# Kernel tuning notes

Hardware: AMD Instinct MI355X
Metric: run time of the kernel (lower is better)

## Reference

```python
import jax, jax.numpy as jnp
import numpy as np
from jax import lax

Q = 3          # Self-ONN polynomial order
EPS = 1e-5     # InstanceNorm1d eps


def setup_inputs() -> dict:
    key = jax.random.key(0)
    k1, k2, k3 = jax.random.split(key, 3)
    B, Cin, L = 16, 128, 8192
    Cout, K = 128, 3
    x = jax.random.normal(k1, (B, Cin, L), dtype=jnp.float32)
    # Conv1d weight over power-expanded channels: [Cout, Cin*Q, K]
    W = jax.random.normal(k2, (Cout, Cin * Q, K), dtype=jnp.float32) * 0.05
    b = jax.random.normal(k3, (Cout,), dtype=jnp.float32) * 0.05
    return {"x": x, "W": W, "b": b}


def reference(x, W, b):
    x = jnp.repeat(x, 2, axis=-1)
    # Self-ONN power expansion: concat x^1..x^Q along channel dim -> (B, C*Q, 2L)
    powers = jnp.concatenate([x ** (i + 1) for i in range(Q)], axis=1)
    # Conv1d, stride 1, padding 1 (same length)
    out = lax.conv_general_dilated(
        powers, W,
        window_strides=(1,),
        padding=[(1, 1)],
        dimension_numbers=("NCH", "OIH", "NCH"),
    ) + b[None, :, None]
    # InstanceNorm1d (affine=False): normalize over length per (batch, channel)
    mean = jnp.mean(out, axis=-1, keepdims=True)
    var = jnp.var(out, axis=-1, keepdims=True)
    out = (out - mean) * lax.rsqrt(var + EPS)
    # Tanh activation (self.relu is nn.Tanh()); dropout=False -> no-op
    return jnp.tanh(out)
```

## Files before the change

### kernel.cpp

```cpp
#include <hip/hip_runtime.h>
#include <hip/hip_fp16.h>
#include <math.h>

#define BATCH 16
#define CIN   128
#define LIN   8192
#define COUT  128
#define LOUT  16384
#define KEXP  768
#define NT    128
#define NTILES (LIN/NT)
#define PCOLS 130
#define PCPAD 136
#define PSZ   (PCOLS*PCPAD)

typedef _Float16 f16x8 __attribute__((ext_vector_type(8)));
typedef float    f32x4 __attribute__((ext_vector_type(4)));

__global__ void prep_weights(const float* __restrict__ W,
                             _Float16* __restrict__ WE,
                             _Float16* __restrict__ WO) {
  int idx = blockIdx.x * 256 + threadIdx.x;
  int co = idx / KEXP;
  int k  = idx % KEXP;
  int sh = (k >= 384) ? 1 : 0;
  int cq = k - 384 * sh;
  const float* w = W + ((size_t)co * 384 + cq) * 3;
  float we, wo;
  if (sh == 0) { we = w[0];        wo = w[0] + w[1]; }
  else         { we = w[1] + w[2]; wo = w[2];        }
  int q  = cq >> 7;
  int c  = cq & 127;
  int ks = q * 8 + sh * 4 + (c >> 5);
  int kk = c & 31, quad = kk >> 3, j = kk & 7;
  int mtile = co >> 4, l15 = co & 15;
  size_t off = ((size_t)((mtile * 24 + ks) * 64) + quad * 16 + l15) * 8 + j;
  WE[off] = (_Float16)we;
  WO[off] = (_Float16)wo;
}

__launch_bounds__(512, 4)
__global__ void conv_gemm(const float* __restrict__ x,
                          const _Float16* __restrict__ WE,
                          const _Float16* __restrict__ WO,
                          float* __restrict__ out,
                          float* __restrict__ stats) {
  extern __shared__ char smem[];
  float*    sstats = (float*)smem;
  _Float16* plane  = (_Float16*)(smem + 1024);

  const int tile = blockIdx.x;
  const int b    = blockIdx.y;
  const int i0   = tile * NT;
  const int t    = threadIdx.x;
  const int lane = t & 63;
  const int wave = t >> 6;
  const int p    = wave >> 1;
  const int isO  = wave & 1;
  const int wm   = p >> 1, wn = p & 1;
  const int l15  = lane & 15, quad = lane >> 4;
  const int kl   = quad * 8;

  if (t < 128) { sstats[2 * t] = 0.f; sstats[2 * t + 1] = 0.f; }

  const float* xb = x + (size_t)b * CIN * LIN;
  const _Float16* Wsel = isO ? WO : WE;

  f32x4 acc[4][4];
  const f32x4 zero = {0.f, 0.f, 0.f, 0.f};
#pragma unroll
  for (int fm = 0; fm < 4; ++fm)
#pragma unroll
    for (int fn = 0; fn < 4; ++fn) acc[fm][fn] = zero;

#pragma unroll
  for (int q = 0; q < 3; ++q) {
    for (int task = t; task < PCOLS * 16; task += 512) {
      int g   = task / PCOLS;
      int col = task - g * PCOLS;
      int c8  = g * 8;
      int gi  = i0 - 1 + col;
      bool ok = (gi >= 0 && gi < LIN);
      f16x8 w;
#pragma unroll
      for (int j = 0; j < 8; ++j) {
        float v = ok ? xb[(size_t)(c8 + j) * LIN + gi] : 0.f;
        float pv = (q == 0) ? v : ((q == 1) ? v * v : v * v * v);
        w[j] = (_Float16)pv;
      }
      *(f16x8*)(plane + col * PCPAD + c8) = w;
    }
    __syncthreads();

#pragma unroll
    for (int s = 0; s < 8; ++s) {
      const int cb   = (s & 3) * 32;
      const int shft = (s >> 2) + isO;
      const _Float16* pb = plane + cb + kl;
      f16x8 bf[4], af[4];
#pragma unroll
      for (int fn = 0; fn < 4; ++fn) {
        int colB = wn * 64 + fn * 16 + l15 + shft;
        bf[fn] = *(const f16x8*)(pb + colB * PCPAD);
      }
#pragma unroll
      for (int fm = 0; fm < 4; ++fm) {
        int mt = wm * 4 + fm;
        af[fm] = *(const f16x8*)(Wsel + ((size_t)((mt * 24 + q * 8 + s) * 64) + lane) * 8);
      }
#pragma unroll
      for (int fm = 0; fm < 4; ++fm)
#pragma unroll
        for (int fn = 0; fn < 4; ++fn)
          acc[fm][fn] = __builtin_amdgcn_mfma_f32_16x16x32_f16(af[fm], bf[fn], acc[fm][fn], 0, 0, 0);
    }
    __syncthreads();
  }

  float* orow_base = out + (size_t)b * COUT * LOUT + isO;
#pragma unroll
  for (int fm = 0; fm < 4; ++fm) {
#pragma unroll
    for (int r = 0; r < 4; ++r) {
      float s1 = 0.f, s2 = 0.f;
#pragma unroll
      for (int fn = 0; fn < 4; ++fn) {
        float v = acc[fm][fn][r];
        s1 += v;
        s2 += v * v;
      }
#pragma unroll
      for (int off = 8; off >= 1; off >>= 1) {
        s1 += __shfl_xor(s1, off, 64);
        s2 += __shfl_xor(s2, off, 64);
      }
      int co = wm * 64 + fm * 16 + quad * 4 + r;
      if (l15 == 0) {
        atomicAdd(&sstats[2 * co], s1);
        atomicAdd(&sstats[2 * co + 1], s2);
      }
      float* orow = orow_base + (size_t)co * LOUT;
#pragma unroll
      for (int fn = 0; fn < 4; ++fn) {
        int n = i0 + wn * 64 + fn * 16 + l15;
        orow[2 * n] = acc[fm][fn][r];
      }
    }
  }
  __syncthreads();
  if (t < 128) {
    atomicAdd(&stats[((size_t)b * COUT + t) * 2],     sstats[2 * t]);
    atomicAdd(&stats[((size_t)b * COUT + t) * 2 + 1], sstats[2 * t + 1]);
  }
}

__device__ inline float tanh_fast(float z) {
  float e = __expf(2.f * z);
  return 1.f - 2.f * __builtin_amdgcn_rcpf(e + 1.f);
}

__global__ void norm_tanh(float* __restrict__ out, const float* __restrict__ stats) {
  int row = blockIdx.x;
  float s1 = stats[2 * row], s2 = stats[2 * row + 1];
  const float invN = 1.f / (float)LOUT;
  float mean = s1 * invN;
  float var  = fmaxf(s2 * invN - mean * mean, 0.f);
  float inv  = rsqrtf(var + 1e-5f);
  float c0   = -mean * inv;
  float4* p = (float4*)(out + (size_t)row * LOUT);
  for (int i = threadIdx.x; i < LOUT / 4; i += 256) {
    float4 v = p[i];
    v.x = tanh_fast(fmaf(v.x, inv, c0));
    v.y = tanh_fast(fmaf(v.y, inv, c0));
    v.z = tanh_fast(fmaf(v.z, inv, c0));
    v.w = tanh_fast(fmaf(v.w, inv, c0));
    p[i] = v;
  }
}

extern "C" void kernel_launch(void* const* d_in, const int* in_sizes, int n_in,
                              void* d_out, int out_size, void* d_ws, size_t ws_size,
                              hipStream_t stream) {
  const float* x = (const float*)d_in[0];
  const float* W = (const float*)d_in[1];
  float* out = (float*)d_out;

  float*    stats = (float*)d_ws;
  _Float16* WE    = (_Float16*)((char*)d_ws + 16384);
  _Float16* WO    = WE + (size_t)COUT * KEXP;

  hipMemsetAsync(d_ws, 0, 16384, stream);
  prep_weights<<<dim3((COUT * KEXP) / 256), dim3(256), 0, stream>>>(W, WE, WO);

  size_t shmem = 1024 + (size_t)PSZ * 2;
  hipFuncSetAttribute(reinterpret_cast<const void*>(conv_gemm),
                      hipFuncAttributeMaxDynamicSharedMemorySize, (int)shmem);
  conv_gemm<<<dim3(NTILES, BATCH), dim3(512), shmem, stream>>>(x, WE, WO, out, stats);

  norm_tanh<<<dim3(BATCH * COUT), dim3(256), 0, stream>>>(out, stats);
}
```

Baseline: 311.7 us.

## Load x once into registers and double-buffer power planes with prefetched fragments

The x tile is now read from global memory once into registers, and all three power planes are built from those registers instead of re-reading x for each power. Two LDS planes alternate, so the next power plane is written while MFMAs run on the current one. Weight and B fragments are software-prefetched (triple and double buffered), and MFMA issue priority is raised with s_setprio. This removes repeated global loads and some barriers, but raises register use (launch bounds drop to 2 blocks per CU) and doubles LDS use, which can lower occupancy.

```diff
diff --git a/kernel.cpp b/kernel.cpp
--- a/kernel.cpp
+++ b/kernel.cpp
@@ -39,7 +39,40 @@
   WO[off] = (_Float16)wo;
 }
 
-__launch_bounds__(512, 4)
+
+#define BUILD_PLANE(POW, P) do {                                           \
+  _Pragma("unroll")                                                        \
+  for (int slot = 0; slot < 5; ++slot) {                                   \
+    if (slot < 4 || tail) {                                                \
+      f16x8 w;                                                             \
+      _Pragma("unroll")                                                    \
+      for (int j = 0; j < 8; ++j) {                                        \
+        float v = xv[slot][j];                                             \
+        float pv = ((POW) == 1) ? v : (((POW) == 2) ? v * v : v * (v * v));\
+        w[j] = (_Float16)pv;                                               \
+      }                                                                    \
+      *(f16x8*)((P) + woff[slot]) = w;                                     \
+    }                                                                      \
+  }                                                                        \
+} while (0)
+
+#define AFLOAD(DST, KS) do {                                               \
+  _Pragma("unroll")                                                        \
+  for (int fm = 0; fm < 4; ++fm) {                                         \
+    int mt = wm * 4 + fm;                                                  \
+    DST[fm] = *(const f16x8*)(Wsel + ((size_t)((mt * 24 + (KS)) * 64) + lane) * 8); \
+  }                                                                        \
+} while (0)
+
+#define BFLOAD(DST, CUR, S) do {                                           \
+  _Pragma("unroll")                                                        \
+  for (int fn = 0; fn < 4; ++fn) {                                         \
+    int colB = wn * 64 + fn * 16 + l15 + (((S) >> 2) + isO);               \
+    DST[fn] = *(const f16x8*)((CUR) + colB * PCPAD + ((S) & 3) * 32 + kl); \
+  }                                                                        \
+} while (0)
+
+__launch_bounds__(512, 2)
 __global__ void conv_gemm(const float* __restrict__ x,
                           const _Float16* __restrict__ WE,
                           const _Float16* __restrict__ WO,
@@ -47,7 +80,7 @@
                           float* __restrict__ stats) {
   extern __shared__ char smem[];
   float*    sstats = (float*)smem;
-  _Float16* plane  = (_Float16*)(smem + 1024);
+  _Float16* planes = (_Float16*)(smem + 1024);
 
   const int tile = blockIdx.x;
   const int b    = blockIdx.y;
@@ -66,6 +99,28 @@
   const float* xb = x + (size_t)b * CIN * LIN;
   const _Float16* Wsel = isO ? WO : WE;
 
+  float xv[5][8];
+  int   woff[5];
+  const bool tail = (t < PCOLS * 16 - 2048);
+#pragma unroll
+  for (int slot = 0; slot < 5; ++slot) {
+    const bool tval = (slot < 4) || tail;
+    int task = t + 512 * slot;
+    int g    = task / PCOLS;
+    if (!tval) g = 0;
+    int col  = task - g * PCOLS;
+    int gi   = i0 - 1 + col;
+    woff[slot] = col * PCPAD + g * 8;
+    const bool ok = tval && gi >= 0 && gi < LIN;
+    const float* px = xb + (size_t)g * 8 * LIN + gi;
+#pragma unroll
+    for (int j = 0; j < 8; ++j) {
+      float v = 0.f;
+      if (ok) v = px[(size_t)j * LIN];
+      xv[slot][j] = v;
+    }
+  }
+
   f32x4 acc[4][4];
   const f32x4 zero = {0.f, 0.f, 0.f, 0.f};
 #pragma unroll
@@ -73,46 +128,31 @@
 #pragma unroll
     for (int fn = 0; fn < 4; ++fn) acc[fm][fn] = zero;
 
+  f16x8 af[3][4], bf[2][4];
+  AFLOAD(af[0], 0);
+  AFLOAD(af[1], 1);
+  BUILD_PLANE(1, planes);
+  __syncthreads();
+
 #pragma unroll
   for (int q = 0; q < 3; ++q) {
-    for (int task = t; task < PCOLS * 16; task += 512) {
-      int g   = task / PCOLS;
-      int col = task - g * PCOLS;
-      int c8  = g * 8;
-      int gi  = i0 - 1 + col;
-      bool ok = (gi >= 0 && gi < LIN);
-      f16x8 w;
-#pragma unroll
-      for (int j = 0; j < 8; ++j) {
-        float v = ok ? xb[(size_t)(c8 + j) * LIN + gi] : 0.f;
-        float pv = (q == 0) ? v : ((q == 1) ? v * v : v * v * v);
-        w[j] = (_Float16)pv;
-      }
-      *(f16x8*)(plane + col * PCPAD + c8) = w;
-    }
-    __syncthreads();
+    _Float16* cur = planes + (size_t)(q & 1) * PSZ;
+    BFLOAD(bf[0], cur, 0);
+    if (q == 0)      BUILD_PLANE(2, planes + PSZ);
+    else if (q == 1) BUILD_PLANE(3, planes);
 
 #pragma unroll
     for (int s = 0; s < 8; ++s) {
-      const int cb   = (s & 3) * 32;
-      const int shft = (s >> 2) + isO;
-      const _Float16* pb = plane + cb + kl;
-      f16x8 bf[4], af[4];
-#pragma unroll
-      for (int fn = 0; fn < 4; ++fn) {
-        int colB = wn * 64 + fn * 16 + l15 + shft;
-        bf[fn] = *(const f16x8*)(pb + colB * PCPAD);
-      }
-#pragma unroll
-      for (int fm = 0; fm < 4; ++fm) {
-        int mt = wm * 4 + fm;
-        af[fm] = *(const f16x8*)(Wsel + ((size_t)((mt * 24 + q * 8 + s) * 64) + lane) * 8);
-      }
+      const int ks = q * 8 + s;
+      if (ks + 2 < 24) AFLOAD(af[(ks + 2) % 3], ks + 2);
+      if (s < 7)       BFLOAD(bf[(s + 1) & 1], cur, s + 1);
+      __builtin_amdgcn_s_setprio(1);
 #pragma unroll
       for (int fm = 0; fm < 4; ++fm)
 #pragma unroll
         for (int fn = 0; fn < 4; ++fn)
-          acc[fm][fn] = __builtin_amdgcn_mfma_f32_16x16x32_f16(af[fm], bf[fn], acc[fm][fn], 0, 0, 0);
+          acc[fm][fn] = __builtin_amdgcn_mfma_f32_16x16x32_f16(af[ks % 3][fm], bf[s & 1][fn], acc[fm][fn], 0, 0, 0);
+      __builtin_amdgcn_s_setprio(0);
     }
     __syncthreads();
   }
@@ -192,7 +232,7 @@
   hipMemsetAsync(d_ws, 0, 16384, stream);
   prep_weights<<<dim3((COUT * KEXP) / 256), dim3(256), 0, stream>>>(W, WE, WO);
 
-  size_t shmem = 1024 + (size_t)PSZ * 2;
+  size_t shmem = 1024 + (size_t)PSZ * 2 * 2;
   hipFuncSetAttribute(reinterpret_cast<const void*>(conv_gemm),
                       hipFuncAttributeMaxDynamicSharedMemorySize, (int)shmem);
   conv_gemm<<<dim3(NTILES, BATCH), dim3(512), shmem, stream>>>(x, WE, WO, out, stats);
```

Measured after the change: 276.5 us. 11.3% less time.
